# Kernel tuning notes

Measured on AMD Instinct MI355X. Metric: run time of the kernel, lower is better.

## Reference

```python
import jax, jax.numpy as jnp
import numpy as np

B, W, R, D = 2, 4096, 8, 32


def setup_inputs() -> dict:
    key = jax.random.key(0)
    k1, k2, k3 = jax.random.split(key, 3)
    q_alpha = jax.random.normal(k1, (B, W, R), dtype=jnp.float32)
    k = jax.random.normal(k2, (B, W, R), dtype=jnp.float32)
    h_norm = jax.random.normal(k3, (B, W, D), dtype=jnp.float32)
    # RetNet-style decay rates per rank channel: gamma_i = 1 - 2^{-(6+i)} in (0, 1)
    gamma_vec = 1.0 - jnp.exp2(-(6.0 + jnp.arange(R, dtype=jnp.float32)))
    idx = jnp.arange(W)
    decay_diff = (idx[:, None] - idx[None, :]).astype(jnp.float32)  # [W, W], i - j
    causal_mask = (idx[:, None] >= idx[None, :]).astype(jnp.float32)  # [W, W] lower-tri
    return {
        "q_alpha": q_alpha,
        "k": k,
        "h_norm": h_norm,
        "gamma_vec": gamma_vec,
        "causal_mask": causal_mask,
        "decay_diff": decay_diff,
    }


def reference(q_alpha, k, h_norm, gamma_vec, causal_mask, decay_diff):
    # q_alpha, k: [B, W, R]; h_norm: [B, W, D]; gamma_vec: [R]; masks: [W, W]
    window = h_norm.shape[1]
    kh = k[..., :, None] * h_norm[..., None, :]  # [B, W, R, D]
    dist = decay_diff[:window, :window][..., None]  # [W, W, 1]
    log_gamma = jnp.log(jnp.clip(gamma_vec, 1e-8, None)).reshape(1, 1, -1)  # [1, 1, R]
    causal = causal_mask[:window, :window][..., None]  # [W, W, 1]
    decay_mask = jnp.exp(dist * log_gamma) * causal  # [W, W, R]
    causal_inner = jnp.einsum("ijr,bjrd->bird", decay_mask, kh)  # [B, W, R, D]
    return jnp.einsum("bwr,bwrd->bwd", q_alpha, causal_inner)  # [B, W, D]
```

## Files before the change

### kernel.cpp

```cpp
#include <hip/hip_runtime.h>

#define B 2
#define W 4096
#define R 8
#define D 32
#define L 64
#define C (W / L)

__device__ __forceinline__ float gamma_of(int r) {
    return 1.0f - exp2f(-(6.0f + (float)r));
}

__global__ __launch_bounds__(256) void k_local(const float* __restrict__ kin,
                                               const float* __restrict__ hin,
                                               float* __restrict__ ws_state) {
    __shared__ float sk[L][R];
    __shared__ float sh[L][D];
    const int blk = blockIdx.x;
    const int b = blk / C, c = blk % C;
    const int t = threadIdx.x;
    const float* kp = kin + ((size_t)b * W + (size_t)c * L) * R;
    const float* hp = hin + ((size_t)b * W + (size_t)c * L) * D;
    if (t < 128) ((float4*)&sk[0][0])[t] = ((const float4*)kp)[t];
    ((float4*)&sh[0][0])[t]       = ((const float4*)hp)[t];
    ((float4*)&sh[0][0])[t + 256] = ((const float4*)hp)[t + 256];
    __syncthreads();
    const int r = t >> 5;
    const int d = t & 31;
    const float g = gamma_of(r);
    float S = 0.f;
#pragma unroll
    for (int j = 0; j < L; ++j) {
        S = S * g + sk[j][r] * sh[j][d];
    }
    ws_state[(size_t)(b * C + c) * (R * D) + t] = S;
}

__global__ __launch_bounds__(256) void k_out(const float* __restrict__ qin,
                                             const float* __restrict__ kin,
                                             const float* __restrict__ hin,
                                             const float* __restrict__ ws_state,
                                             float* __restrict__ out) {
    __shared__ float sq[L][R];
    __shared__ float sk[L][R];
    __shared__ float sh[L][D];
    __shared__ float sA[L][L];
    __shared__ float spow[R][L + 1];
    __shared__ float s0[R][D];
    const int blk = blockIdx.x;
    const int b = blk / C, c = blk % C;
    const int t = threadIdx.x;
    const size_t row0 = (size_t)b * W + (size_t)c * L;
    const float* qp = qin + row0 * R;
    const float* kp = kin + row0 * R;
    const float* hp = hin + row0 * D;
    if (t < 128) {
        ((float4*)&sq[0][0])[t] = ((const float4*)qp)[t];
    } else {
        ((float4*)&sk[0][0])[t - 128] = ((const float4*)kp)[t - 128];
    }
    ((float4*)&sh[0][0])[t]       = ((const float4*)hp)[t];
    ((float4*)&sh[0][0])[t + 256] = ((const float4*)hp)[t + 256];
    if (t < R) {
        const float g = gamma_of(t);
        float p = 1.f;
        for (int dl = 0; dl <= L; ++dl) { spow[t][dl] = p; p *= g; }
    }

    {
        const int r = t >> 5;
        float g = gamma_of(r);
        float gL = g;
#pragma unroll
        for (int s = 0; s < 6; ++s) gL *= gL;
        float P = 0.f;
        const float* wsb = ws_state + (size_t)b * C * (R * D) + t;
        for (int cp = 0; cp < c; ++cp) P = P * gL + wsb[(size_t)cp * (R * D)];
        s0[r][t & 31] = P;
    }
    __syncthreads();

    for (int e = t; e < L * L; e += 256) {
        const int i = e >> 6, j = e & 63;
        float a = 0.f;
        if (j <= i) {
#pragma unroll
            for (int r = 0; r < R; ++r) a += sq[i][r] * sk[j][r] * spow[r][i - j];
        }
        sA[i][j] = a;
    }
    __syncthreads();

    const int d = t & 31;
    const int ig = t >> 5;
    float acc[8];
#pragma unroll
    for (int s = 0; s < 8; ++s) {
        const int i = ig * 8 + s;
        float a = 0.f;
#pragma unroll
        for (int r = 0; r < R; ++r) a += sq[i][r] * spow[r][i + 1] * s0[r][d];
        acc[s] = a;
    }
    for (int j = 0; j < L; ++j) {
        const float hv = sh[j][d];
#pragma unroll
        for (int s = 0; s < 8; ++s) acc[s] += sA[ig * 8 + s][j] * hv;
    }
#pragma unroll
    for (int s = 0; s < 8; ++s) {
        const int i = ig * 8 + s;
        out[(row0 + (size_t)i) * D + d] = acc[s];
    }
}

extern "C" void kernel_launch(void* const* d_in, const int* in_sizes, int n_in,
                              void* d_out, int out_size, void* d_ws, size_t ws_size,
                              hipStream_t stream) {
    const float* q  = (const float*)d_in[0];
    const float* k  = (const float*)d_in[1];
    const float* h  = (const float*)d_in[2];
    float* out = (float*)d_out;
    float* ws  = (float*)d_ws;

    k_local<<<B * C, 256, 0, stream>>>(k, h, ws);
    k_out  <<<B * C, 256, 0, stream>>>(q, k, h, ws, out);
}
```

Measured before the change: 152.7 us.

## Fuse chunk-state and output kernels into one cooperative launch with grid sync

```diff
diff --git a/kernel.cpp b/kernel.cpp
--- a/kernel.cpp
+++ b/kernel.cpp
@@ -1,4 +1,6 @@
 #include <hip/hip_runtime.h>
+#include <hip/hip_cooperative_groups.h>
+namespace cg = cooperative_groups;
 
 #define B 2
 #define W 4096
@@ -11,36 +13,11 @@
     return 1.0f - exp2f(-(6.0f + (float)r));
 }
 
-__global__ __launch_bounds__(256) void k_local(const float* __restrict__ kin,
+__global__ __launch_bounds__(256) void k_fused(const float* __restrict__ qin,
+                                               const float* __restrict__ kin,
                                                const float* __restrict__ hin,
-                                               float* __restrict__ ws_state) {
-    __shared__ float sk[L][R];
-    __shared__ float sh[L][D];
-    const int blk = blockIdx.x;
-    const int b = blk / C, c = blk % C;
-    const int t = threadIdx.x;
-    const float* kp = kin + ((size_t)b * W + (size_t)c * L) * R;
-    const float* hp = hin + ((size_t)b * W + (size_t)c * L) * D;
-    if (t < 128) ((float4*)&sk[0][0])[t] = ((const float4*)kp)[t];
-    ((float4*)&sh[0][0])[t]       = ((const float4*)hp)[t];
-    ((float4*)&sh[0][0])[t + 256] = ((const float4*)hp)[t + 256];
-    __syncthreads();
-    const int r = t >> 5;
-    const int d = t & 31;
-    const float g = gamma_of(r);
-    float S = 0.f;
-#pragma unroll
-    for (int j = 0; j < L; ++j) {
-        S = S * g + sk[j][r] * sh[j][d];
-    }
-    ws_state[(size_t)(b * C + c) * (R * D) + t] = S;
-}
-
-__global__ __launch_bounds__(256) void k_out(const float* __restrict__ qin,
-                                             const float* __restrict__ kin,
-                                             const float* __restrict__ hin,
-                                             const float* __restrict__ ws_state,
-                                             float* __restrict__ out) {
+                                               float* __restrict__ ws_state,
+                                               float* __restrict__ out) {
     __shared__ float sq[L][R];
     __shared__ float sk[L][R];
     __shared__ float sh[L][D];
@@ -54,6 +31,7 @@
     const float* qp = qin + row0 * R;
     const float* kp = kin + row0 * R;
     const float* hp = hin + row0 * D;
+
     if (t < 128) {
         ((float4*)&sq[0][0])[t] = ((const float4*)qp)[t];
     } else {
@@ -66,32 +44,42 @@
         float p = 1.f;
         for (int dl = 0; dl <= L; ++dl) { spow[t][dl] = p; p *= g; }
     }
+    __syncthreads();
+
+    const int r = t >> 5;
+    const int d = t & 31;
+    const float g = gamma_of(r);
+    {
+        float S = 0.f;
+#pragma unroll
+        for (int j = 0; j < L; ++j) S = S * g + sk[j][r] * sh[j][d];
+        ws_state[(size_t)blk * (R * D) + t] = S;
+    }
+
+    for (int e = t; e < L * L; e += 256) {
+        const int i = e >> 6, j = e & 63;
+        float a = 0.f;
+        if (j <= i) {
+#pragma unroll
+            for (int rr = 0; rr < R; ++rr) a += sq[i][rr] * sk[j][rr] * spow[rr][i - j];
+        }
+        sA[i][j] = a;
+    }
+
+    __threadfence();
+    cg::this_grid().sync();
 
     {
-        const int r = t >> 5;
-        float g = gamma_of(r);
         float gL = g;
 #pragma unroll
         for (int s = 0; s < 6; ++s) gL *= gL;
         float P = 0.f;
         const float* wsb = ws_state + (size_t)b * C * (R * D) + t;
         for (int cp = 0; cp < c; ++cp) P = P * gL + wsb[(size_t)cp * (R * D)];
-        s0[r][t & 31] = P;
+        s0[r][d] = P;
     }
     __syncthreads();
 
-    for (int e = t; e < L * L; e += 256) {
-        const int i = e >> 6, j = e & 63;
-        float a = 0.f;
-        if (j <= i) {
-#pragma unroll
-            for (int r = 0; r < R; ++r) a += sq[i][r] * sk[j][r] * spow[r][i - j];
-        }
-        sA[i][j] = a;
-    }
-    __syncthreads();
-
-    const int d = t & 31;
     const int ig = t >> 5;
     float acc[8];
 #pragma unroll
@@ -99,7 +87,7 @@
         const int i = ig * 8 + s;
         float a = 0.f;
 #pragma unroll
-        for (int r = 0; r < R; ++r) a += sq[i][r] * spow[r][i + 1] * s0[r][d];
+        for (int rr = 0; rr < R; ++rr) a += sq[i][rr] * spow[rr][i + 1] * s0[rr][d];
         acc[s] = a;
     }
     for (int j = 0; j < L; ++j) {
@@ -123,6 +111,7 @@
     float* out = (float*)d_out;
     float* ws  = (float*)d_ws;
 
-    k_local<<<B * C, 256, 0, stream>>>(k, h, ws);
-    k_out  <<<B * C, 256, 0, stream>>>(q, k, h, ws, out);
+    void* args[] = { (void*)&q, (void*)&k, (void*)&h, (void*)&ws, (void*)&out };
+    hipLaunchCooperativeKernel((const void*)k_fused, dim3(B * C), dim3(256),
+                               args, 0, stream);
 }
```

Result: slower. 187.8 us (+23.0%).
